# Optimization experiments

Hardware: AMD Instinct MI355X
Metric: run time of the kernel (lower is better)

The kernel has to match this reference:

```python
import jax, jax.numpy as jnp
import numpy as np

MARGIN = 1.0
EPS = 1e-6
DIAG_BIG = 99999.0


def setup_inputs() -> dict:
    key = jax.random.key(0)
    x = jax.random.normal(key, (16384, 256), dtype=jnp.float32)
    # HardNet descriptors are unit-L2 normalized (the distance formula assumes it)
    x = x / jnp.linalg.norm(x, axis=1, keepdims=True)
    return {"x": x}


def reference(x) -> jnp.ndarray:
    cnt = x.shape[0] // 2
    a = x[:cnt]          # [N, d] anchors
    p = x[cnt:]          # [N, d] positives
    # pairwise unit-L2 distance: sqrt((1 - a.p^T + eps) * 2)
    dmat = jnp.sqrt((1.0 - jnp.matmul(a, p.T) + EPS) * 2.0)  # [N, N]
    pos = jnp.diagonal(dmat)                                  # [N]
    # mask diagonal with large constant, then row/col mins = hard negatives
    masked = dmat + jnp.eye(cnt, dtype=dmat.dtype) * DIAG_BIG
    min_a = jnp.min(masked, axis=0)   # best negative anchor per positive
    min_p = jnp.min(masked, axis=1)   # best negative positive per anchor
    neg = jnp.minimum(min_a, min_p)   # [N]
    return jnp.mean(jnp.clip(MARGIN - neg + pos, 0.0))
```

## Files before the change

### kernel.cpp

```cpp
#include <hip/hip_runtime.h>
#include <hip/hip_fp8.h>


#define CNT    8192
#define KDIM   256
#define BIGF   3.0e38f
#define SCALE1 0x7F7F7F7F

typedef float f32x4  __attribute__((ext_vector_type(4)));
typedef float f32x16 __attribute__((ext_vector_type(16)));
typedef int   v8i    __attribute__((ext_vector_type(8)));

union frag8 { uint4 q[2]; v8i v; };

__device__ __forceinline__ unsigned short f2bf(float f) {
    unsigned u = __float_as_uint(f);
    u += 0x7FFFu + ((u >> 16) & 1u);
    return (unsigned short)(u >> 16);
}

__device__ __forceinline__ unsigned cvt4_fp8(float a, float b, float c, float d) {
#if __has_builtin(__builtin_amdgcn_cvt_pk_fp8_f32)
    unsigned v = __builtin_amdgcn_cvt_pk_fp8_f32(a, b, 0, false);
    v = __builtin_amdgcn_cvt_pk_fp8_f32(c, d, v, true);
    return v;
#else
    return (unsigned)__hip_fp8_e4m3(a).__x |
           ((unsigned)__hip_fp8_e4m3(b).__x << 8) |
           ((unsigned)__hip_fp8_e4m3(c).__x << 16) |
           ((unsigned)__hip_fp8_e4m3(d).__x << 24);
#endif
}


__global__ __launch_bounds__(256) void convert_mx_kernel(
    const float* __restrict__ x, unsigned char* __restrict__ xb)
{
    int T    = blockIdx.x * 256 + threadIdx.x;
    int lane = T & 63;
    int h    = (T >> 6) & 1;
    int c    = T >> 7;
    int kc64 = c & 3;
    int rg   = c >> 2;
    int row  = rg * 32 + (lane & 31);
    int col0 = kc64 * 64 + (lane >> 5) * 32 + h * 16;
    const float* src = x + (size_t)row * KDIM + col0;
    float4 u0 = *(const float4*)(src);
    float4 u1 = *(const float4*)(src + 4);
    float4 u2 = *(const float4*)(src + 8);
    float4 u3 = *(const float4*)(src + 12);
    uint4 w;
    w.x = cvt4_fp8(u0.x, u0.y, u0.z, u0.w);
    w.y = cvt4_fp8(u1.x, u1.y, u1.z, u1.w);
    w.z = cvt4_fp8(u2.x, u2.y, u2.z, u2.w);
    w.w = cvt4_fp8(u3.x, u3.y, u3.z, u3.w);
    *(uint4*)(xb + (size_t)T * 16) = w;
}

__device__ __forceinline__ void stage_P(
    const char* __restrict__ Pb, char* lbuf, int bn, int wave, int lane)
{
    #pragma unroll
    for (int t = 0; t < 16; t++) {
        const int o   = wave * 16 + t;
        const int cc  = o >> 1;
        const int h   = o & 1;
        const int rg  = cc & 7;
        const int kcs = cc >> 3;
        const char* src = Pb + (((size_t)(bn * 8 + rg)) << 13)
                             + kcs * 2048 + h * 1024 + lane * 16;
        __builtin_amdgcn_global_load_lds(
            (const __attribute__((address_space(1))) void*)src,
            (__attribute__((address_space(3))) void*)(lbuf + cc * 2048 + h * 1024),
            16, 0, 0);
    }
}

#define TST  136
__global__ __launch_bounds__(256, 2) void dist15_kernel(
    const unsigned char* __restrict__ Ab_, const unsigned char* __restrict__ Pb_,
    float* __restrict__ rowpart, float* __restrict__ colpart,
    float* __restrict__ g_pos)
{
    __shared__ char smem[65536];

    const char* Ab = (const char*)Ab_;
    const char* Pb = (const char*)Pb_;

    const int tid  = threadIdx.x;
    const int l    = blockIdx.x;
    const int xcd  = l & 7;
    const int i    = l >> 3;
    const int bm   = (xcd >> 1) * 16 + (i & 15);
    const int bn   = (xcd & 1) * 16 + (i >> 4);

    const int wave = tid >> 6;
    const int lane = tid & 63;
    const int l31  = lane & 31;
    const int kh   = lane >> 5;
    const int wm   = wave >> 1;
    const int wn   = wave & 1;

    stage_P(Pb, smem, bn, wave, lane);
    __syncthreads();

    f32x16 acc[2][4];
    #pragma unroll
    for (int a = 0; a < 2; a++)
        #pragma unroll
        for (int b = 0; b < 4; b++)
            #pragma unroll
            for (int r = 0; r < 16; r++)
                acc[a][b][r] = 0.f;

    const char* Abase = Ab + lane * 16;
    size_t a_off[2];
    #pragma unroll
    for (int mi = 0; mi < 2; mi++)
        a_off[mi] = (size_t)(bm * 4 + wm * 2 + mi) << 13;

    frag8 ca[2], na[2];
    #pragma unroll
    for (int mi = 0; mi < 2; mi++) {
        ca[mi].q[0] = *(const uint4*)(Abase + a_off[mi]);
        ca[mi].q[1] = *(const uint4*)(Abase + a_off[mi] + 1024);
    }
    #pragma unroll
    for (int kc = 0; kc < 4; kc++) {
        if (kc < 3) {
            #pragma unroll
            for (int mi = 0; mi < 2; mi++) {
                na[mi].q[0] = *(const uint4*)(Abase + a_off[mi] + (kc + 1) * 2048);
                na[mi].q[1] = *(const uint4*)(Abase + a_off[mi] + (kc + 1) * 2048 + 1024);
            }
        }
        frag8 fb[4];
        #pragma unroll
        for (int ni = 0; ni < 4; ni++) {
            const char* p = smem + (kc * 8 + wn * 4 + ni) * 2048 + lane * 16;
            fb[ni].q[0] = *(const uint4*)(p);
            fb[ni].q[1] = *(const uint4*)(p + 1024);
        }
        #pragma unroll
        for (int mi = 0; mi < 2; mi++)
            #pragma unroll
            for (int ni = 0; ni < 4; ni++)
                acc[mi][ni] = __builtin_amdgcn_mfma_scale_f32_32x32x64_f8f6f4(
                    ca[mi].v, fb[ni].v, acc[mi][ni],
                    0, 0,
                    0, SCALE1,
                    0, SCALE1);
        if (kc < 3) {
            #pragma unroll
            for (int mi = 0; mi < 2; mi++) ca[mi] = na[mi];
        }
    }


    if ((bm >> 1) == bn) {
        const int dstart = (bm & 1) * 128;
        #pragma unroll
        for (int mi = 0; mi < 2; mi++)
            #pragma unroll
            for (int ni = 0; ni < 4; ni++)
                #pragma unroll
                for (int reg = 0; reg < 16; reg++) {
                    int rl = wm * 64 + mi * 32 + (reg & 3) + 8 * (reg >> 2) + 4 * kh;
                    int cl = wn * 128 + ni * 32 + l31;
                    if (cl == rl + dstart) {
                        g_pos[bm * 128 + rl] = (1.0f - acc[mi][ni][reg] + 1e-6f) * 2.0f;
                        acc[mi][ni][reg] = -BIGF;
                    }
                }
    }

    #pragma unroll
    for (int ni = 0; ni < 4; ni++) {
        float v = -BIGF;
        #pragma unroll
        for (int mi = 0; mi < 2; mi++)
            #pragma unroll
            for (int reg = 0; reg < 16; reg++)
                v = fmaxf(v, acc[mi][ni][reg]);
        v = fmaxf(v, __shfl_xor(v, 32, 64));
        if (kh == 0) {
            float tt = fmaxf((1.0f - v + 1e-6f) * 2.0f, 0.0f);
            colpart[bm * (2 * CNT / 2) + bn * 256 + wn * 128 + ni * 32 + l31] = tt;
        }
    }

    __syncthreads();
    float* T = (float*)smem;
    const int entry = wn * 32 + l31;
    #pragma unroll
    for (int mi = 0; mi < 2; mi++)
        #pragma unroll
        for (int q = 0; q < 4; q++) {
            f32x4 v;
            #pragma unroll
            for (int rr = 0; rr < 4; rr++) {
                float m = acc[mi][0][q * 4 + rr];
                #pragma unroll
                for (int ni = 1; ni < 4; ni++)
                    m = fmaxf(m, acc[mi][ni][q * 4 + rr]);
                v[rr] = m;
            }
            *(f32x4*)&T[entry * TST + wm * 64 + mi * 32 + q * 8 + kh * 4] = v;
        }
    __syncthreads();

    if (tid < 128) {
        int row = tid;
        float v0 = T[row], v1 = T[TST + row];
        #pragma unroll
        for (int e = 2; e < 64; e += 2) {
            v0 = fmaxf(v0, T[e * TST + row]);
            v1 = fmaxf(v1, T[(e + 1) * TST + row]);
        }
        float v = fmaxf(v0, v1);
        float tt = fmaxf((1.0f - v + 1e-6f) * 2.0f, 0.0f);
        rowpart[bn * CNT + bm * 128 + row] = tt;
    }
}

__global__ __launch_bounds__(256) void finalize1_kernel(
    const float* __restrict__ rowpart, const float* __restrict__ colpart,
    const float* __restrict__ post, float* __restrict__ psum)
{
    const int i = blockIdx.x * 256 + threadIdx.x;
    float rv = BIGF, cv = BIGF;
    #pragma unroll
    for (int bn = 0; bn < 32; bn++)
        rv = fminf(rv, rowpart[bn * CNT + i]);
    #pragma unroll
    for (int bm = 0; bm < 64; bm++)
        cv = fminf(cv, colpart[bm * CNT + i]);
    float t   = fminf(rv, cv);
    float neg = sqrtf(fmaxf(t, 0.f));
    float pos = sqrtf(fmaxf(post[i], 0.f));
    float local = fmaxf(1.0f - neg + pos, 0.0f);
    #pragma unroll
    for (int m = 1; m < 64; m <<= 1) local += __shfl_xor(local, m, 64);
    __shared__ float wsum[4];
    if ((threadIdx.x & 63) == 0) wsum[threadIdx.x >> 6] = local;
    __syncthreads();
    if (threadIdx.x == 0)
        psum[blockIdx.x] = wsum[0] + wsum[1] + wsum[2] + wsum[3];
}

__global__ __launch_bounds__(64) void finalize2_kernel(
    const float* __restrict__ psum, float* __restrict__ out)
{
    float local = (threadIdx.x < 32) ? psum[threadIdx.x] : 0.f;
    #pragma unroll
    for (int m = 1; m < 64; m <<= 1) local += __shfl_xor(local, m, 64);
    if (threadIdx.x == 0) out[0] = local * (1.0f / (float)CNT);
}


#define BM 128
#define BN 128
#define BK 64
#define KST (BK + 8)

typedef __bf16 bf16x8 __attribute__((ext_vector_type(8)));

__global__ __launch_bounds__(256) void init_min_kernel(unsigned* buf, int n) {
    int i = blockIdx.x * 256 + threadIdx.x;
    if (i < n) buf[i] = 0x7F7FFFFFu;
}

__global__ __launch_bounds__(256) void dist_tile_kernel(
    const float* __restrict__ A, const float* __restrict__ P,
    unsigned* __restrict__ g_rowmin, unsigned* __restrict__ g_colmin,
    float* __restrict__ g_pos)
{
    __shared__ unsigned short As[BM * KST];
    __shared__ unsigned short Bs[BN * KST];
    __shared__ unsigned redrow[BM];
    __shared__ unsigned redcol[BN];

    const int tid  = threadIdx.x;
    const int bm   = blockIdx.y;
    const int bn   = blockIdx.x;
    const int wave = tid >> 6;
    const int lane = tid & 63;
    const int quad = lane >> 4;
    const int l15  = lane & 15;
    const int m_off = (wave >> 1) * 64;
    const int n_off = (wave & 1) * 64;

    if (tid < BM) redrow[tid] = 0x7F7FFFFFu;
    if (tid < BN) redcol[tid] = 0x7F7FFFFFu;

    f32x4 acc[4][4];
    #pragma unroll
    for (int i = 0; i < 4; i++)
        #pragma unroll
        for (int j = 0; j < 4; j++)
            acc[i][j] = (f32x4){0.f, 0.f, 0.f, 0.f};

    const int srow = tid >> 4;
    const int scol = tid & 15;

    for (int kc = 0; kc < KDIM / BK; kc++) {
        #pragma unroll
        for (int i = 0; i < 8; i++) {
            int r = srow + i * 16;
            float4 va = *(const float4*)(A + (size_t)(bm * BM + r) * KDIM + kc * BK + scol * 4);
            float4 vb = *(const float4*)(P + (size_t)(bn * BN + r) * KDIM + kc * BK + scol * 4);
            ushort4 wa, wb;
            wa.x = f2bf(va.x); wa.y = f2bf(va.y); wa.z = f2bf(va.z); wa.w = f2bf(va.w);
            wb.x = f2bf(vb.x); wb.y = f2bf(vb.y); wb.z = f2bf(vb.z); wb.w = f2bf(vb.w);
            *(ushort4*)(&As[r * KST + scol * 4]) = wa;
            *(ushort4*)(&Bs[r * KST + scol * 4]) = wb;
        }
        __syncthreads();
        #pragma unroll
        for (int ks = 0; ks < BK / 32; ks++) {
            bf16x8 af[4], bfr[4];
            #pragma unroll
            for (int mi = 0; mi < 4; mi++)
                af[mi] = *(const bf16x8*)(&As[(m_off + mi * 16 + l15) * KST + ks * 32 + quad * 8]);
            #pragma unroll
            for (int ni = 0; ni < 4; ni++)
                bfr[ni] = *(const bf16x8*)(&Bs[(n_off + ni * 16 + l15) * KST + ks * 32 + quad * 8]);
            #pragma unroll
            for (int mi = 0; mi < 4; mi++)
                #pragma unroll
                for (int ni = 0; ni < 4; ni++)
                    acc[mi][ni] = __builtin_amdgcn_mfma_f32_16x16x32_bf16(
                        af[mi], bfr[ni], acc[mi][ni], 0, 0, 0);
        }
        __syncthreads();
    }

    float rmin[4][4], cmin[4];
    #pragma unroll
    for (int mi = 0; mi < 4; mi++)
        #pragma unroll
        for (int r = 0; r < 4; r++) rmin[mi][r] = BIGF;
    #pragma unroll
    for (int ni = 0; ni < 4; ni++) cmin[ni] = BIGF;

    const int grow0 = bm * BM + m_off + quad * 4;
    const int gcol0 = bn * BN + n_off + l15;

    #pragma unroll
    for (int mi = 0; mi < 4; mi++)
        #pragma unroll
        for (int ni = 0; ni < 4; ni++) {
            int gcol = gcol0 + ni * 16;
            #pragma unroll
            for (int r = 0; r < 4; r++) {
                int grow = grow0 + mi * 16 + r;
                float s = acc[mi][ni][r];
                float d = sqrtf((1.0f - s + 1e-6f) * 2.0f);
                float dm = d;
                if (grow == gcol) { g_pos[grow] = d; dm = BIGF; }
                rmin[mi][r] = fminf(rmin[mi][r], dm);
                cmin[ni]    = fminf(cmin[ni], dm);
            }
        }

    #pragma unroll
    for (int mi = 0; mi < 4; mi++)
        #pragma unroll
        for (int r = 0; r < 4; r++) {
            float v = rmin[mi][r];
            v = fminf(v, __shfl_xor(v, 1, 64));
            v = fminf(v, __shfl_xor(v, 2, 64));
            v = fminf(v, __shfl_xor(v, 4, 64));
            v = fminf(v, __shfl_xor(v, 8, 64));
            rmin[mi][r] = v;
        }
    #pragma unroll
    for (int ni = 0; ni < 4; ni++) {
        float v = cmin[ni];
        v = fminf(v, __shfl_xor(v, 16, 64));
        v = fminf(v, __shfl_xor(v, 32, 64));
        cmin[ni] = v;
    }

    if (l15 == 0) {
        #pragma unroll
        for (int mi = 0; mi < 4; mi++)
            #pragma unroll
            for (int r = 0; r < 4; r++)
                atomicMin(&redrow[m_off + mi * 16 + quad * 4 + r],
                          __float_as_uint(rmin[mi][r]));
    }
    if (quad == 0) {
        #pragma unroll
        for (int ni = 0; ni < 4; ni++)
            atomicMin(&redcol[n_off + ni * 16 + l15], __float_as_uint(cmin[ni]));
    }
    __syncthreads();

    if (tid < 128) atomicMin(&g_rowmin[bm * BM + tid], redrow[tid]);
    else           atomicMin(&g_colmin[bn * BN + (tid - 128)], redcol[tid - 128]);
}

__global__ __launch_bounds__(1024) void finalize_kernel(
    const unsigned* __restrict__ g_rowmin, const unsigned* __restrict__ g_colmin,
    const float* __restrict__ g_pos, float* __restrict__ out)
{
    float local = 0.f;
    for (int i = threadIdx.x; i < CNT; i += 1024) {
        float neg = fminf(__uint_as_float(g_rowmin[i]), __uint_as_float(g_colmin[i]));
        float v = 1.0f - neg + g_pos[i];
        local += fmaxf(v, 0.0f);
    }
    #pragma unroll
    for (int m = 1; m < 64; m <<= 1) local += __shfl_xor(local, m, 64);
    __shared__ float wsum[16];
    if ((threadIdx.x & 63) == 0) wsum[threadIdx.x >> 6] = local;
    __syncthreads();
    if (threadIdx.x == 0) {
        float s = 0.f;
        #pragma unroll
        for (int w = 0; w < 16; w++) s += wsum[w];
        out[0] = s * (1.0f / (float)CNT);
    }
}


extern "C" void kernel_launch(void* const* d_in, const int* in_sizes, int n_in,
                              void* d_out, int out_size, void* d_ws, size_t ws_size,
                              hipStream_t stream) {
    const float* x = (const float*)d_in[0];
    float* out = (float*)d_out;

    const size_t fp8_bytes = (size_t)2 * CNT * KDIM;
    const size_t part_f    = (size_t)(32 + 64) * CNT;
    const size_t need = fp8_bytes + part_f * 4 + (size_t)CNT * 4 + 32 * 4;

    if (ws_size >= need) {
        unsigned char* xb      = (unsigned char*)d_ws;
        float*         rowpart = (float*)((char*)d_ws + fp8_bytes);
        float*         colpart = rowpart + (size_t)32 * CNT;
        float*         pos     = colpart + (size_t)64 * CNT;
        float*         psum    = pos + CNT;
        convert_mx_kernel<<<dim3(1024), dim3(256), 0, stream>>>(x, xb);
        dist15_kernel<<<dim3(2048), dim3(256), 0, stream>>>(
            xb, xb + (size_t)CNT * KDIM, rowpart, colpart, pos);
        finalize1_kernel<<<dim3(32), dim3(256), 0, stream>>>(
            rowpart, colpart, pos, psum);
        finalize2_kernel<<<dim3(1), dim3(64), 0, stream>>>(psum, out);
    } else {
        unsigned* rowmin = (unsigned*)d_ws;
        unsigned* colmin = rowmin + CNT;
        float*    pos    = (float*)(colmin + CNT);
        init_min_kernel<<<dim3(2 * CNT / 256), dim3(256), 0, stream>>>(rowmin, 2 * CNT);
        dist_tile_kernel<<<dim3(CNT / BN, CNT / BM), dim3(256), 0, stream>>>(
            x, x + (size_t)CNT * KDIM, rowmin, colmin, pos);
        finalize_kernel<<<dim3(1), dim3(1024), 0, stream>>>(rowmin, colmin, pos, out);
    }
}
```

Measured before the change: 91.80 us.

## Shrink distance tiles to 128x128 with shuffle-based row reductions

The tile drops from 128x256 to 128x128 per block, so the grid doubles to 4096 blocks. LDS usage is halved and launch bounds are raised to 4 blocks per CU, which should raise occupancy. The LDS transpose pass for row maxima is replaced by cross-lane shuffles that write per-wave partials, which removes two barriers. The cost is more partial rows: 128 each for rows and columns, so the finalize kernel reads more data. Register prefetch of A fragments is also removed.

```diff
diff --git a/kernel.cpp b/kernel.cpp
--- a/kernel.cpp
+++ b/kernel.cpp
@@ -57,32 +57,12 @@
     *(uint4*)(xb + (size_t)T * 16) = w;
 }
 
-__device__ __forceinline__ void stage_P(
-    const char* __restrict__ Pb, char* lbuf, int bn, int wave, int lane)
-{
-    #pragma unroll
-    for (int t = 0; t < 16; t++) {
-        const int o   = wave * 16 + t;
-        const int cc  = o >> 1;
-        const int h   = o & 1;
-        const int rg  = cc & 7;
-        const int kcs = cc >> 3;
-        const char* src = Pb + (((size_t)(bn * 8 + rg)) << 13)
-                             + kcs * 2048 + h * 1024 + lane * 16;
-        __builtin_amdgcn_global_load_lds(
-            (const __attribute__((address_space(1))) void*)src,
-            (__attribute__((address_space(3))) void*)(lbuf + cc * 2048 + h * 1024),
-            16, 0, 0);
-    }
-}
-
-#define TST  136
-__global__ __launch_bounds__(256, 2) void dist15_kernel(
+__global__ __launch_bounds__(256, 4) void dist16_kernel(
     const unsigned char* __restrict__ Ab_, const unsigned char* __restrict__ Pb_,
     float* __restrict__ rowpart, float* __restrict__ colpart,
     float* __restrict__ g_pos)
 {
-    __shared__ char smem[65536];
+    __shared__ char smem[32768];
 
     const char* Ab = (const char*)Ab_;
     const char* Pb = (const char*)Pb_;
@@ -91,8 +71,8 @@
     const int l    = blockIdx.x;
     const int xcd  = l & 7;
     const int i    = l >> 3;
-    const int bm   = (xcd >> 1) * 16 + (i & 15);
-    const int bn   = (xcd & 1) * 16 + (i >> 4);
+    const int bm2  = xcd * 8 + (i & 7);
+    const int bn2  = i >> 3;
 
     const int wave = tid >> 6;
     const int lane = tid & 63;
@@ -101,14 +81,27 @@
     const int wm   = wave >> 1;
     const int wn   = wave & 1;
 
-    stage_P(Pb, smem, bn, wave, lane);
+    #pragma unroll
+    for (int t = 0; t < 8; t++) {
+        const int o   = wave * 8 + t;
+        const int cc  = o >> 1;
+        const int h   = o & 1;
+        const int rgl = cc & 3;
+        const int kcs = cc >> 2;
+        const char* src = Pb + (((size_t)(bn2 * 4 + rgl)) << 13)
+                             + kcs * 2048 + h * 1024 + lane * 16;
+        __builtin_amdgcn_global_load_lds(
+            (const __attribute__((address_space(1))) void*)src,
+            (__attribute__((address_space(3))) void*)(smem + cc * 2048 + h * 1024),
+            16, 0, 0);
+    }
     __syncthreads();
 
-    f32x16 acc[2][4];
+    f32x16 acc[2][2];
     #pragma unroll
     for (int a = 0; a < 2; a++)
         #pragma unroll
-        for (int b = 0; b < 4; b++)
+        for (int b = 0; b < 2; b++)
             #pragma unroll
             for (int r = 0; r < 16; r++)
                 acc[a][b][r] = 0.f;
@@ -117,65 +110,52 @@
     size_t a_off[2];
     #pragma unroll
     for (int mi = 0; mi < 2; mi++)
-        a_off[mi] = (size_t)(bm * 4 + wm * 2 + mi) << 13;
-
-    frag8 ca[2], na[2];
-    #pragma unroll
-    for (int mi = 0; mi < 2; mi++) {
-        ca[mi].q[0] = *(const uint4*)(Abase + a_off[mi]);
-        ca[mi].q[1] = *(const uint4*)(Abase + a_off[mi] + 1024);
-    }
+        a_off[mi] = (size_t)(bm2 * 4 + wm * 2 + mi) << 13;
+
     #pragma unroll
     for (int kc = 0; kc < 4; kc++) {
-        if (kc < 3) {
-            #pragma unroll
-            for (int mi = 0; mi < 2; mi++) {
-                na[mi].q[0] = *(const uint4*)(Abase + a_off[mi] + (kc + 1) * 2048);
-                na[mi].q[1] = *(const uint4*)(Abase + a_off[mi] + (kc + 1) * 2048 + 1024);
-            }
-        }
-        frag8 fb[4];
-        #pragma unroll
-        for (int ni = 0; ni < 4; ni++) {
-            const char* p = smem + (kc * 8 + wn * 4 + ni) * 2048 + lane * 16;
+        frag8 fa[2], fb[2];
+        #pragma unroll
+        for (int mi = 0; mi < 2; mi++) {
+            fa[mi].q[0] = *(const uint4*)(Abase + a_off[mi] + kc * 2048);
+            fa[mi].q[1] = *(const uint4*)(Abase + a_off[mi] + kc * 2048 + 1024);
+        }
+        #pragma unroll
+        for (int ni = 0; ni < 2; ni++) {
+            const char* p = smem + (kc * 4 + wn * 2 + ni) * 2048 + lane * 16;
             fb[ni].q[0] = *(const uint4*)(p);
             fb[ni].q[1] = *(const uint4*)(p + 1024);
         }
         #pragma unroll
         for (int mi = 0; mi < 2; mi++)
             #pragma unroll
-            for (int ni = 0; ni < 4; ni++)
+            for (int ni = 0; ni < 2; ni++)
                 acc[mi][ni] = __builtin_amdgcn_mfma_scale_f32_32x32x64_f8f6f4(
-                    ca[mi].v, fb[ni].v, acc[mi][ni],
+                    fa[mi].v, fb[ni].v, acc[mi][ni],
                     0, 0,
                     0, SCALE1,
                     0, SCALE1);
-        if (kc < 3) {
-            #pragma unroll
-            for (int mi = 0; mi < 2; mi++) ca[mi] = na[mi];
-        }
-    }
-
-
-    if ((bm >> 1) == bn) {
-        const int dstart = (bm & 1) * 128;
+    }
+
+
+    if (bm2 == bn2) {
         #pragma unroll
         for (int mi = 0; mi < 2; mi++)
             #pragma unroll
-            for (int ni = 0; ni < 4; ni++)
+            for (int ni = 0; ni < 2; ni++)
                 #pragma unroll
                 for (int reg = 0; reg < 16; reg++) {
                     int rl = wm * 64 + mi * 32 + (reg & 3) + 8 * (reg >> 2) + 4 * kh;
-                    int cl = wn * 128 + ni * 32 + l31;
-                    if (cl == rl + dstart) {
-                        g_pos[bm * 128 + rl] = (1.0f - acc[mi][ni][reg] + 1e-6f) * 2.0f;
+                    int cl = wn * 64 + ni * 32 + l31;
+                    if (cl == rl) {
+                        g_pos[bm2 * 128 + rl] = (1.0f - acc[mi][ni][reg] + 1e-6f) * 2.0f;
                         acc[mi][ni][reg] = -BIGF;
                     }
                 }
     }
 
     #pragma unroll
-    for (int ni = 0; ni < 4; ni++) {
+    for (int ni = 0; ni < 2; ni++) {
         float v = -BIGF;
         #pragma unroll
         for (int mi = 0; mi < 2; mi++)
@@ -185,42 +165,27 @@
         v = fmaxf(v, __shfl_xor(v, 32, 64));
         if (kh == 0) {
             float tt = fmaxf((1.0f - v + 1e-6f) * 2.0f, 0.0f);
-            colpart[bm * (2 * CNT / 2) + bn * 256 + wn * 128 + ni * 32 + l31] = tt;
-        }
-    }
-
-    __syncthreads();
-    float* T = (float*)smem;
-    const int entry = wn * 32 + l31;
+            colpart[(size_t)(bm2 * 2 + wm) * CNT
+                    + bn2 * 128 + wn * 64 + ni * 32 + l31] = tt;
+        }
+    }
+
     #pragma unroll
     for (int mi = 0; mi < 2; mi++)
         #pragma unroll
-        for (int q = 0; q < 4; q++) {
-            f32x4 v;
-            #pragma unroll
-            for (int rr = 0; rr < 4; rr++) {
-                float m = acc[mi][0][q * 4 + rr];
-                #pragma unroll
-                for (int ni = 1; ni < 4; ni++)
-                    m = fmaxf(m, acc[mi][ni][q * 4 + rr]);
-                v[rr] = m;
+        for (int reg = 0; reg < 16; reg++) {
+            float v = fmaxf(acc[mi][0][reg], acc[mi][1][reg]);
+            v = fmaxf(v, __shfl_xor(v, 1, 64));
+            v = fmaxf(v, __shfl_xor(v, 2, 64));
+            v = fmaxf(v, __shfl_xor(v, 4, 64));
+            v = fmaxf(v, __shfl_xor(v, 8, 64));
+            v = fmaxf(v, __shfl_xor(v, 16, 64));
+            if (l31 == 0) {
+                int rl = wm * 64 + mi * 32 + (reg & 3) + 8 * (reg >> 2) + 4 * kh;
+                float tt = fmaxf((1.0f - v + 1e-6f) * 2.0f, 0.0f);
+                rowpart[(size_t)(bn2 * 2 + wn) * CNT + bm2 * 128 + rl] = tt;
             }
-            *(f32x4*)&T[entry * TST + wm * 64 + mi * 32 + q * 8 + kh * 4] = v;
-        }
-    __syncthreads();
-
-    if (tid < 128) {
-        int row = tid;
-        float v0 = T[row], v1 = T[TST + row];
-        #pragma unroll
-        for (int e = 2; e < 64; e += 2) {
-            v0 = fmaxf(v0, T[e * TST + row]);
-            v1 = fmaxf(v1, T[(e + 1) * TST + row]);
-        }
-        float v = fmaxf(v0, v1);
-        float tt = fmaxf((1.0f - v + 1e-6f) * 2.0f, 0.0f);
-        rowpart[bn * CNT + bm * 128 + row] = tt;
-    }
+        }
 }
 
 __global__ __launch_bounds__(256) void finalize1_kernel(
@@ -229,12 +194,12 @@
 {
     const int i = blockIdx.x * 256 + threadIdx.x;
     float rv = BIGF, cv = BIGF;
-    #pragma unroll
-    for (int bn = 0; bn < 32; bn++)
-        rv = fminf(rv, rowpart[bn * CNT + i]);
-    #pragma unroll
-    for (int bm = 0; bm < 64; bm++)
-        cv = fminf(cv, colpart[bm * CNT + i]);
+    #pragma unroll 8
+    for (int s = 0; s < 128; s++)
+        rv = fminf(rv, rowpart[(size_t)s * CNT + i]);
+    #pragma unroll 8
+    for (int s = 0; s < 128; s++)
+        cv = fminf(cv, colpart[(size_t)s * CNT + i]);
     float t   = fminf(rv, cv);
     float neg = sqrtf(fmaxf(t, 0.f));
     float pos = sqrtf(fmaxf(post[i], 0.f));
@@ -432,17 +397,17 @@
     float* out = (float*)d_out;
 
     const size_t fp8_bytes = (size_t)2 * CNT * KDIM;
-    const size_t part_f    = (size_t)(32 + 64) * CNT;
+    const size_t part_f    = (size_t)(128 + 128) * CNT;
     const size_t need = fp8_bytes + part_f * 4 + (size_t)CNT * 4 + 32 * 4;
 
     if (ws_size >= need) {
         unsigned char* xb      = (unsigned char*)d_ws;
         float*         rowpart = (float*)((char*)d_ws + fp8_bytes);
-        float*         colpart = rowpart + (size_t)32 * CNT;
-        float*         pos     = colpart + (size_t)64 * CNT;
+        float*         colpart = rowpart + (size_t)128 * CNT;
+        float*         pos     = colpart + (size_t)128 * CNT;
         float*         psum    = pos + CNT;
         convert_mx_kernel<<<dim3(1024), dim3(256), 0, stream>>>(x, xb);
-        dist15_kernel<<<dim3(2048), dim3(256), 0, stream>>>(
+        dist16_kernel<<<dim3(4096), dim3(256), 0, stream>>>(
             xb, xb + (size_t)CNT * KDIM, rowpart, colpart, pos);
         finalize1_kernel<<<dim3(32), dim3(256), 0, stream>>>(
             rowpart, colpart, pos, psum);
```

After: 194.6 us. 2.12x slower.
